# Optimization experiments

Measured on AMD Instinct MI355X. Metric: run time of the kernel, lower is better.

Reference implementation:

```python
import jax, jax.numpy as jnp
import numpy as np

B, N, K = 32, 64, 128          # batch, atoms per cell, channel width (128x0e + 128x1o)
R_MAX = 5.0
NUM_BESSEL = 8
P_CUT = 5                       # num_polynomial_cutoff
AVG_NEIGH = 16.0                # avg_num_neighbors
H_MLP = 512                     # hidden_dimensions_size, n_hidden_dimensions = 2
FEAT = 5 * K                    # ((num_interactions-1)*4 + 1) * 128 = 640


def silu(x):
    return x * jax.nn.sigmoid(x)


def _bessel_cutoff(r, mask):
    # Bessel radial basis * polynomial cutoff (MACE), masked on valid edges.
    n = jnp.arange(1, NUM_BESSEL + 1, dtype=r.dtype)
    rb = jnp.sqrt(2.0 / R_MAX) * jnp.sin(n * (jnp.pi / R_MAX) * r[..., None]) / r[..., None]
    u = r / R_MAX
    p = float(P_CUT)
    fc = 1.0 - 0.5 * (p + 1) * (p + 2) * u**P_CUT + p * (p + 2) * u**(P_CUT + 1) - 0.5 * p * (p + 1) * u**(P_CUT + 2)
    fc = fc * (u < 1.0)
    return rb * (fc * mask)[..., None]


def _sph(uvec):
    # Real spherical harmonics l=0,1,2 (component normalization), uvec: unit edge vectors.
    x, y, z = uvec[..., 0], uvec[..., 1], uvec[..., 2]
    s3, s5, s15 = 3.0**0.5, 5.0**0.5, 15.0**0.5
    Y0 = jnp.ones_like(x)[..., None]
    Y1 = jnp.stack([s3 * x, s3 * y, s3 * z], -1)
    Y2 = jnp.stack([s15 * x * y, s15 * y * z, 0.5 * s5 * (3 * z * z - 1.0),
                    s15 * x * z, 0.5 * s15 * (x * x - y * y)], -1)
    return Y0, Y1, Y2


def _radial_mlp(x, w0, b0, w1, b1, w2, b2, w3, b3):
    h = silu(x @ w0 + b0)
    h = silu(h @ w1 + b1)
    h = silu(h @ w2 + b2)
    return h @ w3 + b3


def setup_inputs() -> dict:
    key = jax.random.key(0)
    ks = jax.random.split(key, 32)
    f32 = jnp.float32

    def lin(k, fan_in, shape):
        return (jax.random.normal(k, shape, dtype=f32) / np.sqrt(fan_in)).astype(f32)

    inp = {
        "noisy_relative_positions": jax.random.uniform(ks[0], (B, N, 3), dtype=f32),
        "time": jax.random.uniform(ks[1], (B, 1), dtype=f32),
        "unit_cell": (11.0 * jnp.eye(3, dtype=f32) + 0.3 * jax.random.uniform(ks[2], (B, 3, 3), dtype=f32)),
        "w_embed": lin(ks[3], 1, (K,)),
        # interaction 1 radial MLP: 8 -> 64 -> 64 -> 64 -> 3*K (weights for l=0,1,2 paths)
        "r1_w0": lin(ks[4], NUM_BESSEL, (NUM_BESSEL, 64)), "r1_b0": jnp.zeros((64,), f32),
        "r1_w1": lin(ks[5], 64, (64, 64)), "r1_b1": jnp.zeros((64,), f32),
        "r1_w2": lin(ks[6], 64, (64, 64)), "r1_b2": jnp.zeros((64,), f32),
        "r1_w3": lin(ks[7], 64, (64, 3 * K)), "r1_b3": jnp.zeros((3 * K,), f32),
        "mix1_l0": lin(ks[8], K, (K, K)),
        "mix1_l1": lin(ks[9], K, (K, K)),
        "mix1_l2": lin(ks[10], K, (K, K)),
        # interaction 2 radial MLP: 8 -> 64 -> 64 -> 64 -> 2*K (paths 0e x 0e -> 0e, 1o x 1o -> 0e)
        "r2_w0": lin(ks[11], NUM_BESSEL, (NUM_BESSEL, 64)), "r2_b0": jnp.zeros((64,), f32),
        "r2_w1": lin(ks[12], 64, (64, 64)), "r2_b1": jnp.zeros((64,), f32),
        "r2_w2": lin(ks[13], 64, (64, 64)), "r2_b2": jnp.zeros((64,), f32),
        "r2_w3": lin(ks[14], 64, (64, 2 * K)), "r2_b3": jnp.zeros((2 * K,), f32),
        "mix2": lin(ks[15], K, (K, K)),
        # readout MLP: 641 -> 512 -> 512 -> 3
        "mlp_w0": lin(ks[16], FEAT + 1, (FEAT + 1, H_MLP)), "mlp_b0": jnp.zeros((H_MLP,), f32),
        "mlp_w1": lin(ks[17], H_MLP, (H_MLP, H_MLP)), "mlp_b1": jnp.zeros((H_MLP,), f32),
        "mlp_w2": lin(ks[18], H_MLP, (H_MLP, 3)), "mlp_b2": jnp.zeros((3,), f32),
    }
    return inp


def reference(noisy_relative_positions, time, unit_cell, w_embed,
              r1_w0, r1_b0, r1_w1, r1_b1, r1_w2, r1_b2, r1_w3, r1_b3,
              mix1_l0, mix1_l1, mix1_l2,
              r2_w0, r2_b0, r2_w1, r2_b1, r2_w2, r2_b2, r2_w3, r2_b3, mix2,
              mlp_w0, mlp_b0, mlp_w1, mlp_b1, mlp_w2, mlp_b2):
    frac = noisy_relative_positions                      # [B,N,3] fractional
    d = frac[:, :, None, :] - frac[:, None, :, :]        # [B,N,N,3]
    d = d - jnp.round(d)                                 # minimum-image PBC
    dc = jnp.einsum('bijc,bcd->bijd', d, unit_cell)      # cartesian displacements
    r = jnp.sqrt(jnp.maximum(jnp.sum(dc * dc, -1), 1e-12))
    mask = (r < R_MAX) & (~jnp.eye(N, dtype=bool))[None]
    r_safe = jnp.where(mask, r, 1.0)
    uvec = dc / r_safe[..., None] * mask[..., None]      # unit edge vectors (0 off-edge)

    rad = _bessel_cutoff(r_safe, mask)                   # [B,N,N,8]
    Y0, Y1, Y2 = _sph(uvec)                              # [B,N,N,1|3|5]

    h0 = jnp.broadcast_to(w_embed, (B, N, K))            # element embedding (single species)

    # ---- interaction 1: radial-weighted tensor product h_j (x) Y_l, scatter over j ----
    we = _radial_mlp(rad, r1_w0, r1_b0, r1_w1, r1_b1, r1_w2, r1_b2, r1_w3, r1_b3)
    we = we.reshape(B, N, N, 3, K) * mask[..., None, None]
    hj = h0[:, None, :, :]                               # sender features [B,1,N,K]
    msg0 = jnp.einsum('bijk,bijm->bimk', we[..., 0, :] * hj, Y0)[:, :, 0] / AVG_NEIGH  # [B,N,K]
    msg1 = jnp.einsum('bijk,bijm->bimk', we[..., 1, :] * hj, Y1) / AVG_NEIGH           # [B,N,3,K]
    msg2 = jnp.einsum('bijk,bijm->bimk', we[..., 2, :] * hj, Y2) / AVG_NEIGH           # [B,N,5,K]

    s1 = msg0 @ mix1_l0 + jnp.sum(msg2 * msg2, axis=2) @ mix1_l2   # scalars [B,N,K]
    v1 = jnp.einsum('bimk,kc->bimc', msg1, mix1_l1)                # vectors [B,N,3,K]
    h1 = silu(s1)

    # ---- interaction 2: scalar output from 0e x 0e and 1o x 1o -> 0e paths ----
    we2 = _radial_mlp(rad, r2_w0, r2_b0, r2_w1, r2_b1, r2_w2, r2_b2, r2_w3, r2_b3)
    we2 = we2.reshape(B, N, N, 2, K) * mask[..., None, None]
    msg_a = jnp.sum(we2[..., 0, :] * h1[:, None, :, :], axis=2)    # [B,N,K]
    inv = jnp.einsum('bijm,bjmk->bijk', Y1, v1)                    # Y1 . v1_j invariant
    msg_b = jnp.sum(we2[..., 1, :] * inv, axis=2)
    s2 = ((msg_a + msg_b) / AVG_NEIGH) @ mix2                      # [B,N,K]

    # node_feats: layer1 full irreps (128x0e + 128x1o -> 512) + layer2 scalars (128) = 640
    node_feats = jnp.concatenate([s1, v1.reshape(B, N, 3 * K), s2], axis=-1)

    t = jnp.broadcast_to(time[:, None, :], (B, N, 1))
    x = jnp.concatenate([node_feats, t], axis=-1)                  # [B,N,641]
    x = jax.nn.relu(x @ mlp_w0 + mlp_b0)
    x = jax.nn.relu(x @ mlp_w1 + mlp_b1)
    return x @ mlp_w2 + mlp_b2                                     # [B,N,3]
```

## Files before the change

### kernel.cpp

```cpp
#include <hip/hip_runtime.h>
#include <math.h>

#define B_ 32
#define N_ 64
#define K_ 128
#define NPAIR (B_*N_*N_)

typedef __attribute__((ext_vector_type(8))) short short8;
typedef __attribute__((ext_vector_type(8))) __bf16 bf16x8;
typedef __attribute__((ext_vector_type(4))) float floatx4;

__device__ __forceinline__ float silu_f(float x) {
    return x / (1.0f + expf(-x));
}
__device__ __forceinline__ float4 ld4(const float* p) { return *(const float4*)p; }

__device__ __forceinline__ short f2bf(float x) {
    union { float f; unsigned u; } v; v.f = x;
    unsigned r = (v.u + 0x7FFFu + ((v.u >> 16) & 1u)) >> 16;
    return (short)r;
}
__device__ __forceinline__ float bf2f(short s) {
    union { unsigned u; float f; } v;
    v.u = ((unsigned)(unsigned short)s) << 16;
    return v.f;
}
__device__ __forceinline__ bf16x8 ld_frag(const short* p) {
    short8 r = *(const short8*)p;
    return __builtin_bit_cast(bf16x8, r);
}

__global__ __launch_bounds__(256) void prep_kernel(
    const float* __restrict__ r1w0, const float* __restrict__ r1w1,
    const float* __restrict__ r1w2, const float* __restrict__ r1w3,
    const float* __restrict__ r2w0, const float* __restrict__ r2w1,
    const float* __restrict__ r2w2, const float* __restrict__ r2w3,
    const float* __restrict__ r2b3,
    const float* __restrict__ mw0, const float* __restrict__ mw1,
    const float* __restrict__ wemb,
    const float* __restrict__ l0, const float* __restrict__ l1,
    const float* __restrict__ l2, const float* __restrict__ mix2,
    short* __restrict__ dst)
{
    int idx = blockIdx.x * 256 + threadIdx.x;
    if (idx >= 757760) return;
    short v;
    if (idx < 4096) {
        int n = idx >> 6, k = idx & 63; v = f2bf(r1w1[k*64 + n]);
    } else if (idx < 8192) {
        int i = idx - 4096; int n = i >> 6, k = i & 63; v = f2bf(r1w2[k*64 + n]);
    } else if (idx < 12288) {
        int i = idx - 8192; int n = i >> 6, k = i & 63; v = f2bf(r2w1[k*64 + n]);
    } else if (idx < 16384) {
        int i = idx - 12288; int n = i >> 6, k = i & 63; v = f2bf(r2w2[k*64 + n]);
    } else if (idx < 40960) {
        int i = idx - 16384; int col = i / 96, k = i - col*96;
        v = (k < 64) ? f2bf(r2w3[k*256 + col])
          : (k == 64) ? f2bf(r2b3[col]) : (short)0;
    } else if (idx < 401408) {
        int i = idx - 40960; int n = i / 704, k = i - n*704;
        v = (k < 641) ? f2bf(mw0[(size_t)k*512 + n]) : (short)0;
    } else if (idx < 663552) {
        int i = idx - 401408; int n = i >> 9, k = i & 511;
        v = f2bf(mw1[(size_t)k*512 + n]);
    } else if (idx < 665600) {
        int i = idx - 663552; int n = i >> 5, k = i & 31;
        v = (k < 8) ? f2bf(r1w0[k*64 + n]) : (short)0;
    } else if (idx < 667648) {
        int i = idx - 665600; int n = i >> 5, k = i & 31;
        v = (k < 8) ? f2bf(r2w0[k*64 + n]) : (short)0;
    } else if (idx < 692224) {
        int i = idx - 667648; int col = i >> 6, h = i & 63;
        v = f2bf(r1w3[h*384 + col] * wemb[col & 127] * 0.0625f);
    } else if (idx < 741376) {
        int i = idx - 692224; int n = i / 384, k = i - n*384;
        float f;
        if (k < 128)       f = l0[k*128 + n];
        else if (k < 256)  f = l2[(k-128)*128 + n];
        else               f = l1[(k-256)*128 + n];
        v = f2bf(f);
    } else {
        int i = idx - 741376; int n = i >> 7, k = i & 127;
        v = f2bf(mix2[k*128 + n] * 0.0625f);
    }
    dst[idx] = v;
}

__global__ __launch_bounds__(256) void geom_kernel(
    const float* __restrict__ pos, const float* __restrict__ cell,
    short* __restrict__ radbf, float* __restrict__ Y1, float* __restrict__ Y2,
    float* __restrict__ maskf)
{
    int p = blockIdx.x * 256 + threadIdx.x;
    if (p >= NPAIR) return;
    int b = p >> 12;
    int ij = p & 4095;
    int i = ij >> 6, j = ij & 63;
    const float* pi = pos + (size_t)(b*N_ + i)*3;
    const float* pj = pos + (size_t)(b*N_ + j)*3;
    float d0 = pi[0]-pj[0], d1 = pi[1]-pj[1], d2 = pi[2]-pj[2];
    d0 -= rintf(d0); d1 -= rintf(d1); d2 -= rintf(d2);
    const float* C = cell + b*9;
    float dc0 = d0*C[0] + d1*C[3] + d2*C[6];
    float dc1 = d0*C[1] + d1*C[4] + d2*C[7];
    float dc2 = d0*C[2] + d1*C[5] + d2*C[8];
    float r2 = fmaxf(dc0*dc0 + dc1*dc1 + dc2*dc2, 1e-12f);
    float r = sqrtf(r2);
    bool m = (r < 5.0f) && (i != j);
    float mf = m ? 1.0f : 0.0f;
    float rs = m ? r : 1.0f;
    float inv_rs = 1.0f / rs;
    float x = dc0*inv_rs*mf, y = dc1*inv_rs*mf, z = dc2*inv_rs*mf;
    float u = r * 0.2f;
    float u2 = u*u, u4 = u2*u2, u5 = u4*u;
    float fc = 1.0f - 21.0f*u5 + 35.0f*u5*u - 15.0f*u5*u2;
    fc = (u < 1.0f) ? fc : 0.0f;
    float pref = 0.6324555320336759f * inv_rs * (fc * mf);
    float w = 0.6283185307179586f * rs;
    float sw = sinf(w), cw = cosf(w);
    float c2 = 2.0f * cw;
    short8 sv;
    float sp = 0.f, s = sw;
    #pragma unroll
    for (int n = 0; n < 8; n++) {
        sv[n] = f2bf(pref * s);
        float ns = c2*s - sp;
        sp = s; s = ns;
    }
    *(short8*)&radbf[(size_t)p*8] = sv;
    const float s3  = 1.7320508075688772f;
    const float s5  = 2.23606797749979f;
    const float s15 = 3.872983346207417f;
    float* y1 = Y1 + (size_t)p*3;
    y1[0] = s3*x; y1[1] = s3*y; y1[2] = s3*z;
    float* y2 = Y2 + (size_t)p*5;
    y2[0] = s15*x*y;
    y2[1] = s15*y*z;
    y2[2] = 0.5f*s5*(3.0f*z*z - 1.0f);
    y2[3] = s15*x*z;
    y2[4] = 0.5f*s15*(x*x - y*y);
    maskf[p] = mf;
}

__global__ __launch_bounds__(256) void bigmlp_kernel(
    const short* __restrict__ radbf,
    const short* __restrict__ w0T1, const float* __restrict__ b01,
    const short* __restrict__ w1T1, const float* __restrict__ b11,
    const short* __restrict__ w2T1, const float* __restrict__ b21,
    short* __restrict__ hc1,
    const short* __restrict__ w0T2, const float* __restrict__ b02,
    const short* __restrict__ w1T2, const float* __restrict__ b12,
    const short* __restrict__ w2T2, const float* __restrict__ b22,
    short* __restrict__ hc2)
{
    __shared__ short radB[128*40];
    __shared__ short actA[128*72];
    __shared__ short actB[128*72];
    int t = threadIdx.x;
    int wv = t >> 6, lane = t & 63, qd = lane >> 4, nn = lane & 15;
    size_t p0 = (size_t)blockIdx.x * 128;

    if (t < 128) {
        uint4 rv = *(const uint4*)&radbf[(p0 + t)*8];
        uint4 z = {0,0,0,0};
        *(uint4*)&radB[t*40]      = rv;
        *(uint4*)&radB[t*40 + 8]  = z;
        *(uint4*)&radB[t*40 + 16] = z;
        *(uint4*)&radB[t*40 + 24] = z;
        *(uint4*)&radB[t*40 + 32] = z;
    }
    __syncthreads();

    const short* w0Ts[2] = {w0T1, w0T2};
    const short* w1Ts[2] = {w1T1, w1T2};
    const short* w2Ts[2] = {w2T1, w2T2};
    const float* b0s[2]  = {b01, b02};
    const float* b1s[2]  = {b11, b12};
    const float* b2s[2]  = {b21, b22};
    short* hcs[2] = {hc1, hc2};

    for (int net = 0; net < 2; net++) {
        const short* w0T = w0Ts[net];
        const short* w1T = w1Ts[net];
        const short* w2T = w2Ts[net];
        const float* b0 = b0s[net];
        const float* b1 = b1s[net];
        const float* b2 = b2s[net];
        short* hc = hcs[net];
        #pragma unroll
        for (int ms = 0; ms < 2; ms++) {
            int r0 = wv*32 + ms*16;
            bf16x8 a = ld_frag(&radB[(r0 + nn)*40 + qd*8]);
            #pragma unroll
            for (int tt = 0; tt < 4; tt++) {
                floatx4 acc = (floatx4){0.f,0.f,0.f,0.f};
                bf16x8 bb = ld_frag(&w0T[(tt*16 + nn)*32 + qd*8]);
                acc = __builtin_amdgcn_mfma_f32_16x16x32_bf16(a, bb, acc, 0, 0, 0);
                int col = tt*16 + nn;
                float bv = b0[col];
                #pragma unroll
                for (int i = 0; i < 4; i++)
                    actA[(r0 + qd*4 + i)*72 + col] = f2bf(silu_f(acc[i] + bv));
            }
        }
        __syncthreads();
        #pragma unroll
        for (int ms = 0; ms < 2; ms++) {
            int r0 = wv*32 + ms*16;
            bf16x8 a0 = ld_frag(&actA[(r0 + nn)*72 + qd*8]);
            bf16x8 a1 = ld_frag(&actA[(r0 + nn)*72 + 32 + qd*8]);
            #pragma unroll
            for (int tt = 0; tt < 4; tt++) {
                floatx4 acc = (floatx4){0.f,0.f,0.f,0.f};
                bf16x8 b0f = ld_frag(&w1T[(tt*16 + nn)*64 + qd*8]);
                bf16x8 b1f = ld_frag(&w1T[(tt*16 + nn)*64 + 32 + qd*8]);
                acc = __builtin_amdgcn_mfma_f32_16x16x32_bf16(a0, b0f, acc, 0, 0, 0);
                acc = __builtin_amdgcn_mfma_f32_16x16x32_bf16(a1, b1f, acc, 0, 0, 0);
                int col = tt*16 + nn;
                float bv = b1[col];
                #pragma unroll
                for (int i = 0; i < 4; i++)
                    actB[(r0 + qd*4 + i)*72 + col] = f2bf(silu_f(acc[i] + bv));
            }
        }
        __syncthreads();
        #pragma unroll
        for (int ms = 0; ms < 2; ms++) {
            int r0 = wv*32 + ms*16;
            bf16x8 a0 = ld_frag(&actB[(r0 + nn)*72 + qd*8]);
            bf16x8 a1 = ld_frag(&actB[(r0 + nn)*72 + 32 + qd*8]);
            #pragma unroll
            for (int tt = 0; tt < 4; tt++) {
                floatx4 acc = (floatx4){0.f,0.f,0.f,0.f};
                bf16x8 b0f = ld_frag(&w2T[(tt*16 + nn)*64 + qd*8]);
                bf16x8 b1f = ld_frag(&w2T[(tt*16 + nn)*64 + 32 + qd*8]);
                acc = __builtin_amdgcn_mfma_f32_16x16x32_bf16(a0, b0f, acc, 0, 0, 0);
                acc = __builtin_amdgcn_mfma_f32_16x16x32_bf16(a1, b1f, acc, 0, 0, 0);
                int col = tt*16 + nn;
                float bv = b2[col];
                #pragma unroll
                for (int i = 0; i < 4; i++)
                    hc[(p0 + r0 + qd*4 + i)*64 + col] = f2bf(silu_f(acc[i] + bv));
            }
        }
    }
}

__global__ __launch_bounds__(256) void msg1_kernel(
    const short* __restrict__ hc1, const float* __restrict__ Y1g,
    const float* __restrict__ Y2g, const float* __restrict__ maskg,
    const float* __restrict__ wemb, const float* __restrict__ b3,
    const short* __restrict__ w3T, const short* __restrict__ lT,
    const float* __restrict__ timeg,
    short* __restrict__ h1bf, float* __restrict__ v1g, short* __restrict__ featsb)
{
    __shared__ __align__(16) char pool[19008];
    short* hcT  = (short*)pool;
    short* A2   = (short*)pool;
    short* YmB  = (short*)(pool + 9216);
    short* GB   = (short*)(pool + 11520);
    float* msgF = (float*)(pool + 13824);
    float* qF   = (float*)(pool + 18432);
    float* SY   = (float*)(pool + 18944);

    int t = threadIdx.x;
    int wv = t >> 6, lane = t & 63, qd = lane >> 4, nn = lane & 15;
    int node = blockIdx.x;
    int b = node >> 6;
    size_t pbase = (size_t)node * 64;

    for (int idx = t; idx < 512; idx += 256) {
        int j = idx >> 3, h0 = (idx & 7)*8;
        short8 v = *(const short8*)&hc1[((size_t)node*64 + j)*64 + h0];
        #pragma unroll
        for (int q = 0; q < 8; q++) hcT[(h0 + q)*72 + j] = v[q];
    }
    for (int idx = t; idx < 1152; idx += 256) YmB[idx] = 0;
    __syncthreads();
    if (t < 64) {
        int j = t;
        float mf = maskg[pbase + j];
        YmB[j] = f2bf(mf);
        #pragma unroll
        for (int m = 0; m < 3; m++) YmB[(1+m)*72 + j] = f2bf(Y1g[(pbase+j)*3 + m] * mf);
        #pragma unroll
        for (int m = 0; m < 5; m++) YmB[(4+m)*72 + j] = f2bf(Y2g[(pbase+j)*5 + m] * mf);
    }
    __syncthreads();
    if (t < 16) {
        float acc = 0.f;
        if (t < 9) for (int j = 0; j < 64; j++) acc += bf2f(YmB[t*72 + j]);
        SY[t] = acc;
    }
    {
        floatx4 accG = (floatx4){0.f,0.f,0.f,0.f};
        #pragma unroll
        for (int ks = 0; ks < 64; ks += 32) {
            bf16x8 a = ld_frag(&YmB[nn*72 + ks + qd*8]);
            bf16x8 bfr = ld_frag(&hcT[(wv*16 + nn)*72 + ks + qd*8]);
            accG = __builtin_amdgcn_mfma_f32_16x16x32_bf16(a, bfr, accG, 0, 0, 0);
        }
        #pragma unroll
        for (int i = 0; i < 4; i++)
            GB[(qd*4 + i)*72 + wv*16 + nn] = f2bf(accG[i]);
    }
    __syncthreads();
    {
        bf16x8 a0f = ld_frag(&GB[nn*72 + 0  + qd*8]);
        bf16x8 a1f = ld_frag(&GB[nn*72 + 32 + qd*8]);
        #pragma unroll
        for (int tl = 0; tl < 6; tl++) {
            int col0 = (wv*6 + tl)*16;
            floatx4 acc = (floatx4){0.f,0.f,0.f,0.f};
            bf16x8 b0f = ld_frag(&w3T[(col0 + nn)*64 + 0  + qd*8]);
            bf16x8 b1f = ld_frag(&w3T[(col0 + nn)*64 + 32 + qd*8]);
            acc = __builtin_amdgcn_mfma_f32_16x16x32_bf16(a0f, b0f, acc, 0, 0, 0);
            acc = __builtin_amdgcn_mfma_f32_16x16x32_bf16(a1f, b1f, acc, 0, 0, 0);
            int col = col0 + nn;
            int csec = col >> 7, k = col & 127;
            #pragma unroll
            for (int i = 0; i < 4; i++) {
                int m = qd*4 + i;
                bool valid = (csec == 0) ? (m == 0)
                           : (csec == 1) ? (m >= 1 && m <= 3)
                                         : (m >= 4 && m <= 8);
                if (valid)
                    msgF[m*128 + k] = acc[i] + SY[m]*b3[col]*wemb[k]*0.0625f;
            }
        }
    }
    __syncthreads();
    if (t < 128) {
        float acc = 0.f;
        #pragma unroll
        for (int m = 4; m < 9; m++) { float v = msgF[m*128 + t]; acc += v*v; }
        qF[t] = acc;
    }
    __syncthreads();
    for (int idx = t; idx < 6272; idx += 256) A2[idx] = 0;
    __syncthreads();
    A2[t] = (t < 128) ? f2bf(msgF[t]) : f2bf(qF[t - 128]);
    if (t < 128) {
        #pragma unroll
        for (int m = 1; m <= 3; m++)
            A2[m*392 + 256 + t] = f2bf(msgF[m*128 + t]);
    }
    __syncthreads();
    #pragma unroll
    for (int tt = 0; tt < 2; tt++) {
        int col = (wv*2 + tt)*16 + nn;
        floatx4 acc = (floatx4){0.f,0.f,0.f,0.f};
        #pragma unroll
        for (int ks = 0; ks < 384; ks += 32) {
            bf16x8 a = ld_frag(&A2[nn*392 + ks + qd*8]);
            bf16x8 bfr = ld_frag(&lT[(size_t)col*384 + ks + qd*8]);
            acc = __builtin_amdgcn_mfma_f32_16x16x32_bf16(a, bfr, acc, 0, 0, 0);
        }
        if (qd == 0) {
            float s1 = acc[0];
            featsb[(size_t)node*704 + col] = f2bf(s1);
            h1bf[(size_t)node*128 + col] = f2bf(silu_f(s1));
            #pragma unroll
            for (int i = 1; i < 4; i++) {
                float v = acc[i];
                v1g[(size_t)node*384 + (i-1)*128 + col] = v;
                featsb[(size_t)node*704 + 128 + (i-1)*128 + col] = f2bf(v);
            }
        }
    }
    if (t == 0) featsb[(size_t)node*704 + 640] = f2bf(timeg[b]);
    if (t < 63) featsb[(size_t)node*704 + 641 + t] = 0;
}

__global__ __launch_bounds__(256) void msg2_kernel(
    const short* __restrict__ hc2, const float* __restrict__ Y1g,
    const float* __restrict__ maskg, const short* __restrict__ w3extT,
    const short* __restrict__ h1bf, const float* __restrict__ v1g,
    short* __restrict__ msgabf)
{
    __shared__ __align__(16) char pool[50688];
    short* hc2e  = (short*)pool;
    short* h1B   = (short*)(pool + 14336);
    short* invB  = (short*)(pool + 31744);
    float* Y1s   = (float*)(pool + 49152);
    float* msgab = (float*)(pool + 50176);

    int t = threadIdx.x;
    int wv = t >> 6, lane = t & 63, qd = lane >> 4, nn = lane & 15;
    int node = blockIdx.x;
    int b = node >> 6;
    size_t pbase = (size_t)node * 64;

    if (t < 64) {
        int j = t;
        #pragma unroll
        for (int m = 0; m < 3; m++) Y1s[j*4 + m] = Y1g[(pbase+j)*3 + m];
        float mf = maskg[pbase + j];
        short8 z8 = {0,0,0,0,0,0,0,0};
        *(short8*)&hc2e[j*112 + 64] = z8;
        *(short8*)&hc2e[j*112 + 72] = z8;
        *(short8*)&hc2e[j*112 + 80] = z8;
        *(short8*)&hc2e[j*112 + 88] = z8;
        *(short8*)&hc2e[j*112 + 96] = z8;
        *(short8*)&hc2e[j*112 + 104] = z8;
        hc2e[j*112 + 64] = f2bf(mf);
    }
    for (int idx = t; idx < 512; idx += 256) {
        int j = idx >> 3, h0 = (idx & 7)*8;
        short8 v = *(const short8*)&hc2[((size_t)node*64 + j)*64 + h0];
        float mf = maskg[pbase + j];
        if (mf == 0.f) { short8 z8 = {0,0,0,0,0,0,0,0}; v = z8; }
        *(short8*)&hc2e[j*112 + h0] = v;
    }
    for (int idx = t; idx < 1024; idx += 256) {
        int j = idx >> 4, k0 = (idx & 15)*8;
        *(uint4*)&h1B[j*136 + k0] = *(const uint4*)&h1bf[((size_t)b*64 + j)*128 + k0];
    }
    if (t < 128) msgab[t] = 0.f;
    __syncthreads();
    for (int idx = t; idx < 2048; idx += 256) {
        int j = idx >> 5, kq = (idx & 31)*4;
        const float* vb = &v1g[((size_t)b*64 + j)*384 + kq];
        float4 vx = ld4(vb), vy = ld4(vb + 128), vz = ld4(vb + 256);
        float yx = Y1s[j*4+0], yy = Y1s[j*4+1], yz = Y1s[j*4+2];
        invB[j*136 + kq + 0] = f2bf(yx*vx.x + yy*vy.x + yz*vz.x);
        invB[j*136 + kq + 1] = f2bf(yx*vx.y + yy*vy.y + yz*vz.y);
        invB[j*136 + kq + 2] = f2bf(yx*vx.z + yy*vy.z + yz*vz.z);
        invB[j*136 + kq + 3] = f2bf(yx*vx.w + yy*vy.w + yz*vz.w);
    }
    __syncthreads();
    {
        bf16x8 a0 = ld_frag(&hc2e[(wv*16 + nn)*112 + 0  + qd*8]);
        bf16x8 a1 = ld_frag(&hc2e[(wv*16 + nn)*112 + 32 + qd*8]);
        bf16x8 a2 = ld_frag(&hc2e[(wv*16 + nn)*112 + 64 + qd*8]);
        for (int g = 0; g < 4; g++) {
            #pragma unroll
            for (int tt = 0; tt < 4; tt++) {
                int col0 = g*64 + tt*16;
                floatx4 acc = (floatx4){0.f,0.f,0.f,0.f};
                bf16x8 b0f = ld_frag(&w3extT[(col0 + nn)*96 + 0  + qd*8]);
                bf16x8 b1f = ld_frag(&w3extT[(col0 + nn)*96 + 32 + qd*8]);
                bf16x8 b2f = ld_frag(&w3extT[(col0 + nn)*96 + 64 + qd*8]);
                acc = __builtin_amdgcn_mfma_f32_16x16x32_bf16(a0, b0f, acc, 0, 0, 0);
                acc = __builtin_amdgcn_mfma_f32_16x16x32_bf16(a1, b1f, acc, 0, 0, 0);
                acc = __builtin_amdgcn_mfma_f32_16x16x32_bf16(a2, b2f, acc, 0, 0, 0);
                int col = col0 + nn;
                int k = col & 127;
                const short* src = (col < 128) ? h1B : invB;
                float p = 0.f;
                #pragma unroll
                for (int i = 0; i < 4; i++) {
                    int j = wv*16 + qd*4 + i;
                    p += acc[i] * bf2f(src[j*136 + k]);
                }
                p += __shfl_xor(p, 16);
                p += __shfl_xor(p, 32);
                if (qd == 0) atomicAdd(&msgab[k], p);
            }
        }
    }
    __syncthreads();
    if (t < 128) msgabf[(size_t)node*128 + t] = f2bf(msgab[t]);
}

__global__ __launch_bounds__(64) void s2_kernel(
    const short* __restrict__ msgabf, const short* __restrict__ mix2T,
    short* __restrict__ featsb)
{
    int lane = threadIdx.x, qd = lane >> 4, nn = lane & 15;
    int m0 = blockIdx.x * 16, n0 = blockIdx.y * 64;
    floatx4 acc[4];
    #pragma unroll
    for (int tt = 0; tt < 4; tt++) acc[tt] = (floatx4){0.f,0.f,0.f,0.f};
    #pragma unroll
    for (int ks = 0; ks < 128; ks += 32) {
        bf16x8 a = ld_frag(&msgabf[(size_t)(m0 + nn)*128 + ks + qd*8]);
        #pragma unroll
        for (int tt = 0; tt < 4; tt++) {
            bf16x8 bb = ld_frag(&mix2T[(size_t)(n0 + tt*16 + nn)*128 + ks + qd*8]);
            acc[tt] = __builtin_amdgcn_mfma_f32_16x16x32_bf16(a, bb, acc[tt], 0, 0, 0);
        }
    }
    #pragma unroll
    for (int tt = 0; tt < 4; tt++) {
        int n = n0 + tt*16 + nn;
        #pragma unroll
        for (int i = 0; i < 4; i++) {
            int m = m0 + qd*4 + i;
            featsb[(size_t)m*704 + 512 + n] = f2bf(acc[tt][i]);
        }
    }
}

__global__ __launch_bounds__(256) void gemm_part_kernel(
    const short* __restrict__ A, int lda,
    const short* __restrict__ BT, int ldb,
    int ngran, int nsplit, float* __restrict__ Cp)
{
    int t = threadIdx.x;
    int wv = t >> 6, lane = t & 63, qd = lane >> 4, nn = lane & 15;
    int m0 = blockIdx.x * 64, n0 = blockIdx.y * 64, z = blockIdx.z;
    int g0 = (z*ngran)/nsplit, g1 = ((z+1)*ngran)/nsplit;
    floatx4 acc[4];
    #pragma unroll
    for (int tt = 0; tt < 4; tt++) acc[tt] = (floatx4){0.f,0.f,0.f,0.f};
    int row = wv*16 + nn;
    for (int g = g0; g < g1; g++) {
        int k = g*32;
        bf16x8 a = ld_frag(&A[(size_t)(m0 + row)*lda + k + qd*8]);
        #pragma unroll
        for (int tt = 0; tt < 4; tt++) {
            bf16x8 bb = ld_frag(&BT[(size_t)(n0 + tt*16 + nn)*ldb + k + qd*8]);
            acc[tt] = __builtin_amdgcn_mfma_f32_16x16x32_bf16(a, bb, acc[tt], 0, 0, 0);
        }
    }
    float* out = Cp + (size_t)z*2048*512;
    #pragma unroll
    for (int tt = 0; tt < 4; tt++) {
        int n = n0 + tt*16 + nn;
        #pragma unroll
        for (int i = 0; i < 4; i++)
            out[(size_t)(m0 + wv*16 + qd*4 + i)*512 + n] = acc[tt][i];
    }
}

__global__ __launch_bounds__(256) void combine_kernel(
    const float* __restrict__ Cp, const float* __restrict__ bias,
    short* __restrict__ out)
{
    int idx = (blockIdx.x * 256 + threadIdx.x) * 4;
    int n = idx & 511;
    float4 s = ld4(&Cp[idx]);
    #pragma unroll
    for (int z = 1; z < 4; z++) {
        float4 p = ld4(&Cp[(size_t)z*1048576 + idx]);
        s.x += p.x; s.y += p.y; s.z += p.z; s.w += p.w;
    }
    float4 bv = ld4(&bias[n]);
    short4 o;
    o.x = f2bf(fmaxf(s.x + bv.x, 0.f));
    o.y = f2bf(fmaxf(s.y + bv.y, 0.f));
    o.z = f2bf(fmaxf(s.z + bv.z, 0.f));
    o.w = f2bf(fmaxf(s.w + bv.w, 0.f));
    *(short4*)&out[idx] = o;
}

__global__ __launch_bounds__(64) void final3_kernel(
    const short* __restrict__ H, const float* __restrict__ w2,
    const float* __restrict__ b2, float* __restrict__ out)
{
    int node = blockIdx.x, lane = threadIdx.x;
    float a0 = 0.f, a1 = 0.f, a2 = 0.f;
    #pragma unroll
    for (int r = 0; r < 8; r++) {
        int k = r*64 + lane;
        float h = bf2f(H[(size_t)node*512 + k]);
        a0 += h * w2[k*3 + 0];
        a1 += h * w2[k*3 + 1];
        a2 += h * w2[k*3 + 2];
    }
    #pragma unroll
    for (int off = 32; off > 0; off >>= 1) {
        a0 += __shfl_down(a0, off);
        a1 += __shfl_down(a1, off);
        a2 += __shfl_down(a2, off);
    }
    if (lane == 0) {
        out[(size_t)node*3 + 0] = a0 + b2[0];
        out[(size_t)node*3 + 1] = a1 + b2[1];
        out[(size_t)node*3 + 2] = a2 + b2[2];
    }
}

extern "C" void kernel_launch(void* const* d_in, const int* in_sizes, int n_in,
                              void* d_out, int out_size, void* d_ws, size_t ws_size,
                              hipStream_t stream) {
    const float* pos   = (const float*)d_in[0];
    const float* timeg = (const float*)d_in[1];
    const float* cell  = (const float*)d_in[2];
    const float* wemb  = (const float*)d_in[3];
    const float* r1w0  = (const float*)d_in[4];
    const float* r1b0  = (const float*)d_in[5];
    const float* r1w1  = (const float*)d_in[6];
    const float* r1b1  = (const float*)d_in[7];
    const float* r1w2  = (const float*)d_in[8];
    const float* r1b2  = (const float*)d_in[9];
    const float* r1w3  = (const float*)d_in[10];
    const float* r1b3  = (const float*)d_in[11];
    const float* l0    = (const float*)d_in[12];
    const float* l1    = (const float*)d_in[13];
    const float* l2    = (const float*)d_in[14];
    const float* r2w0  = (const float*)d_in[15];
    const float* r2b0  = (const float*)d_in[16];
    const float* r2w1  = (const float*)d_in[17];
    const float* r2b1  = (const float*)d_in[18];
    const float* r2w2  = (const float*)d_in[19];
    const float* r2b2  = (const float*)d_in[20];
    const float* r2w3  = (const float*)d_in[21];
    const float* r2b3  = (const float*)d_in[22];
    const float* mix2  = (const float*)d_in[23];
    const float* mw0   = (const float*)d_in[24];
    const float* mb0   = (const float*)d_in[25];
    const float* mw1   = (const float*)d_in[26];
    const float* mb1   = (const float*)d_in[27];
    const float* mw2   = (const float*)d_in[28];
    const float* mb2   = (const float*)d_in[29];

    float* ws = (float*)d_ws;
    short* radbf  = (short*)ws;
    float* Y1     = ws + 524288;
    float* Y2     = ws + 917504;
    float* maskf  = ws + 1572864;
    float* v1     = ws + 1703936;
    short* featsb = (short*)(ws + 2490368);
    short* prep   = (short*)(ws + 3211264);
    short* hc1    = (short*)(ws + 3590144);
    short* hc2    = (short*)(ws + 7784448);
    short* h1bf   = (short*)(ws + 11978752);
    short* msgabf = (short*)(ws + 12109824);

    short* w1T_1  = prep;
    short* w2T_1  = prep + 4096;
    short* w1T_2  = prep + 8192;
    short* w2T_2  = prep + 12288;
    short* w3extT = prep + 16384;
    short* wT0    = prep + 40960;
    short* wT1    = prep + 401408;
    short* w0T_1  = prep + 663552;
    short* w0T_2  = prep + 665600;
    short* w3T_1  = prep + 667648;
    short* lT     = prep + 692224;
    short* mix2T  = prep + 741376;

    float* Cp   = (float*)hc1;
    short* h0bb = radbf;
    short* h1bb = (short*)Y2;

    prep_kernel<<<(757760 + 255)/256, 256, 0, stream>>>(
        r1w0, r1w1, r1w2, r1w3, r2w0, r2w1, r2w2, r2w3, r2b3,
        mw0, mw1, wemb, l0, l1, l2, mix2, prep);
    geom_kernel<<<NPAIR/256, 256, 0, stream>>>(pos, cell, radbf, Y1, Y2, maskf);
    bigmlp_kernel<<<NPAIR/128, 256, 0, stream>>>(radbf,
        w0T_1, r1b0, w1T_1, r1b1, w2T_1, r1b2, hc1,
        w0T_2, r2b0, w1T_2, r2b1, w2T_2, r2b2, hc2);
    msg1_kernel<<<B_*N_, 256, 0, stream>>>(hc1, Y1, Y2, maskf, wemb, r1b3,
        w3T_1, lT, timeg, h1bf, v1, featsb);
    msg2_kernel<<<B_*N_, 256, 0, stream>>>(hc2, Y1, maskf, w3extT, h1bf, v1,
        msgabf);
    {
        dim3 g(128, 2);
        s2_kernel<<<g, 64, 0, stream>>>(msgabf, mix2T, featsb);
    }
    {
        dim3 g(32, 8, 4);
        gemm_part_kernel<<<g, 256, 0, stream>>>(featsb, 704, wT0, 704, 22, 4, Cp);
        combine_kernel<<<1024, 256, 0, stream>>>(Cp, mb0, h0bb);
        gemm_part_kernel<<<g, 256, 0, stream>>>(h0bb, 512, wT1, 512, 16, 4, Cp);
        combine_kernel<<<1024, 256, 0, stream>>>(Cp, mb1, h1bb);
    }
    final3_kernel<<<B_*N_, 64, 0, stream>>>(h1bb, mw2, mb2, (float*)d_out);
}
```

Before: 322.0 us.

## Exploit pair symmetry, merge geom into prep, fold s2 into msg2

Geometry is computed only for the upper triangle of atom pairs (i<=j), and the mirrored entries are written with Y1 negated and Y2, mask and radial features reused. The radial-MLP kernel now processes only the 2080 triangular pairs per cell and scatters each hidden row to both (i,j) and (j,i). The geometry and weight-prep kernels are merged into one launch. The s2 GEMM kernel is removed in favour of a scalar dot-product loop at the end of msg2, and silu/sin/cos/rcp switch to fast AMD intrinsics. This roughly halves the radial-MLP work and drops two launches, at the cost of scattered writes and a serial 128-step loop per thread in msg2.

```diff
diff --git a/kernel.cpp b/kernel.cpp
--- a/kernel.cpp
+++ b/kernel.cpp
@@ -5,13 +5,18 @@
 #define N_ 64
 #define K_ 128
 #define NPAIR (B_*N_*N_)
+#define NTRI 2080
+#define GEOM_BLOCKS 260
+#define PREP_COUNT 741376
+#define PREP_BLOCKS 2896
 
 typedef __attribute__((ext_vector_type(8))) short short8;
 typedef __attribute__((ext_vector_type(8))) __bf16 bf16x8;
 typedef __attribute__((ext_vector_type(4))) float floatx4;
 
 __device__ __forceinline__ float silu_f(float x) {
-    return x / (1.0f + expf(-x));
+    float e = __builtin_amdgcn_exp2f(-1.442695040888963f * x);
+    return x * __builtin_amdgcn_rcpf(1.0f + e);
 }
 __device__ __forceinline__ float4 ld4(const float* p) { return *(const float4*)p; }
 
@@ -30,7 +35,22 @@
     return __builtin_bit_cast(bf16x8, r);
 }
 
-__global__ __launch_bounds__(256) void prep_kernel(
+__device__ __forceinline__ int2 tri_decode(int t) {
+    float f = (129.0f - sqrtf((float)(16641 - 8*t))) * 0.5f;
+    int i = (int)f;
+    int off = 64*i - (i*(i-1))/2;
+    if (off > t) { i--; off = 64*i - (i*(i-1))/2; }
+    else {
+        int offn = 64*(i+1) - ((i+1)*i)/2;
+        if (offn <= t) { i = i+1; off = offn; }
+    }
+    return make_int2(i, i + (t - off));
+}
+
+__global__ __launch_bounds__(256) void pre_kernel(
+    const float* __restrict__ pos, const float* __restrict__ cell,
+    short* __restrict__ radbf, float* __restrict__ Y1, float* __restrict__ Y2,
+    float* __restrict__ maskf,
     const float* __restrict__ r1w0, const float* __restrict__ r1w1,
     const float* __restrict__ r1w2, const float* __restrict__ r1w3,
     const float* __restrict__ r2w0, const float* __restrict__ r2w1,
@@ -39,11 +59,66 @@
     const float* __restrict__ mw0, const float* __restrict__ mw1,
     const float* __restrict__ wemb,
     const float* __restrict__ l0, const float* __restrict__ l1,
-    const float* __restrict__ l2, const float* __restrict__ mix2,
-    short* __restrict__ dst)
+    const float* __restrict__ l2, short* __restrict__ dst)
 {
-    int idx = blockIdx.x * 256 + threadIdx.x;
-    if (idx >= 757760) return;
+    int t = threadIdx.x;
+    if (blockIdx.x < GEOM_BLOCKS) {
+        int gt = blockIdx.x * 256 + t;
+        int b = gt / NTRI;
+        int tt = gt - b*NTRI;
+        int2 ij = tri_decode(tt);
+        int i = ij.x, j = ij.y;
+        const float* pi = pos + (size_t)(b*N_ + i)*3;
+        const float* pj = pos + (size_t)(b*N_ + j)*3;
+        float d0 = pi[0]-pj[0], d1 = pi[1]-pj[1], d2 = pi[2]-pj[2];
+        d0 -= rintf(d0); d1 -= rintf(d1); d2 -= rintf(d2);
+        const float* C = cell + b*9;
+        float dc0 = d0*C[0] + d1*C[3] + d2*C[6];
+        float dc1 = d0*C[1] + d1*C[4] + d2*C[7];
+        float dc2 = d0*C[2] + d1*C[5] + d2*C[8];
+        float r2 = fmaxf(dc0*dc0 + dc1*dc1 + dc2*dc2, 1e-12f);
+        float r = sqrtf(r2);
+        bool m = (r < 5.0f) && (i != j);
+        float mf = m ? 1.0f : 0.0f;
+        float rs = m ? r : 1.0f;
+        float inv_rs = __builtin_amdgcn_rcpf(rs);
+        inv_rs = inv_rs * (2.0f - rs*inv_rs);
+        float x = dc0*inv_rs*mf, y = dc1*inv_rs*mf, z = dc2*inv_rs*mf;
+        float u = r * 0.2f;
+        float u2 = u*u, u4 = u2*u2, u5 = u4*u;
+        float fc = 1.0f - 21.0f*u5 + 35.0f*u5*u - 15.0f*u5*u2;
+        fc = (u < 1.0f) ? fc : 0.0f;
+        float pref = 0.6324555320336759f * inv_rs * (fc * mf);
+        float rev = 0.1f * rs;
+        float sw = __builtin_amdgcn_sinf(rev);
+        float cw = __builtin_amdgcn_cosf(rev);
+        float c2 = 2.0f * cw;
+        short8 sv;
+        float sp = 0.f, s = sw;
+        #pragma unroll
+        for (int n = 0; n < 8; n++) {
+            sv[n] = f2bf(pref * s);
+            float ns = c2*s - sp;
+            sp = s; s = ns;
+        }
+        size_t pu = ((size_t)b*64 + i)*64 + j;
+        size_t pl = ((size_t)b*64 + j)*64 + i;
+        *(short8*)&radbf[pu*8] = sv;
+        const float s3  = 1.7320508075688772f;
+        const float s5  = 2.23606797749979f;
+        const float s15 = 3.872983346207417f;
+        float y1x = s3*x, y1y = s3*y, y1z = s3*z;
+        Y1[pu*3+0] = y1x; Y1[pu*3+1] = y1y; Y1[pu*3+2] = y1z;
+        Y1[pl*3+0] = -y1x; Y1[pl*3+1] = -y1y; Y1[pl*3+2] = -y1z;
+        float q0 = s15*x*y, q1 = s15*y*z, q2 = 0.5f*s5*(3.0f*z*z - 1.0f);
+        float q3 = s15*x*z, q4 = 0.5f*s15*(x*x - y*y);
+        Y2[pu*5+0]=q0; Y2[pu*5+1]=q1; Y2[pu*5+2]=q2; Y2[pu*5+3]=q3; Y2[pu*5+4]=q4;
+        Y2[pl*5+0]=q0; Y2[pl*5+1]=q1; Y2[pl*5+2]=q2; Y2[pl*5+3]=q3; Y2[pl*5+4]=q4;
+        maskf[pu] = mf; maskf[pl] = mf;
+        return;
+    }
+    int idx = (blockIdx.x - GEOM_BLOCKS) * 256 + t;
+    if (idx >= PREP_COUNT) return;
     short v;
     if (idx < 4096) {
         int n = idx >> 6, k = idx & 63; v = f2bf(r1w1[k*64 + n]);
@@ -72,74 +147,15 @@
     } else if (idx < 692224) {
         int i = idx - 667648; int col = i >> 6, h = i & 63;
         v = f2bf(r1w3[h*384 + col] * wemb[col & 127] * 0.0625f);
-    } else if (idx < 741376) {
+    } else {
         int i = idx - 692224; int n = i / 384, k = i - n*384;
         float f;
         if (k < 128)       f = l0[k*128 + n];
         else if (k < 256)  f = l2[(k-128)*128 + n];
         else               f = l1[(k-256)*128 + n];
         v = f2bf(f);
-    } else {
-        int i = idx - 741376; int n = i >> 7, k = i & 127;
-        v = f2bf(mix2[k*128 + n] * 0.0625f);
     }
     dst[idx] = v;
-}
-
-__global__ __launch_bounds__(256) void geom_kernel(
-    const float* __restrict__ pos, const float* __restrict__ cell,
-    short* __restrict__ radbf, float* __restrict__ Y1, float* __restrict__ Y2,
-    float* __restrict__ maskf)
-{
-    int p = blockIdx.x * 256 + threadIdx.x;
-    if (p >= NPAIR) return;
-    int b = p >> 12;
-    int ij = p & 4095;
-    int i = ij >> 6, j = ij & 63;
-    const float* pi = pos + (size_t)(b*N_ + i)*3;
-    const float* pj = pos + (size_t)(b*N_ + j)*3;
-    float d0 = pi[0]-pj[0], d1 = pi[1]-pj[1], d2 = pi[2]-pj[2];
-    d0 -= rintf(d0); d1 -= rintf(d1); d2 -= rintf(d2);
-    const float* C = cell + b*9;
-    float dc0 = d0*C[0] + d1*C[3] + d2*C[6];
-    float dc1 = d0*C[1] + d1*C[4] + d2*C[7];
-    float dc2 = d0*C[2] + d1*C[5] + d2*C[8];
-    float r2 = fmaxf(dc0*dc0 + dc1*dc1 + dc2*dc2, 1e-12f);
-    float r = sqrtf(r2);
-    bool m = (r < 5.0f) && (i != j);
-    float mf = m ? 1.0f : 0.0f;
-    float rs = m ? r : 1.0f;
-    float inv_rs = 1.0f / rs;
-    float x = dc0*inv_rs*mf, y = dc1*inv_rs*mf, z = dc2*inv_rs*mf;
-    float u = r * 0.2f;
-    float u2 = u*u, u4 = u2*u2, u5 = u4*u;
-    float fc = 1.0f - 21.0f*u5 + 35.0f*u5*u - 15.0f*u5*u2;
-    fc = (u < 1.0f) ? fc : 0.0f;
-    float pref = 0.6324555320336759f * inv_rs * (fc * mf);
-    float w = 0.6283185307179586f * rs;
-    float sw = sinf(w), cw = cosf(w);
-    float c2 = 2.0f * cw;
-    short8 sv;
-    float sp = 0.f, s = sw;
-    #pragma unroll
-    for (int n = 0; n < 8; n++) {
-        sv[n] = f2bf(pref * s);
-        float ns = c2*s - sp;
-        sp = s; s = ns;
-    }
-    *(short8*)&radbf[(size_t)p*8] = sv;
-    const float s3  = 1.7320508075688772f;
-    const float s5  = 2.23606797749979f;
-    const float s15 = 3.872983346207417f;
-    float* y1 = Y1 + (size_t)p*3;
-    y1[0] = s3*x; y1[1] = s3*y; y1[2] = s3*z;
-    float* y2 = Y2 + (size_t)p*5;
-    y2[0] = s15*x*y;
-    y2[1] = s15*y*z;
-    y2[2] = 0.5f*s5*(3.0f*z*z - 1.0f);
-    y2[3] = s15*x*z;
-    y2[4] = 0.5f*s15*(x*x - y*y);
-    maskf[p] = mf;
 }
 
 __global__ __launch_bounds__(256) void bigmlp_kernel(
@@ -156,13 +172,24 @@
     __shared__ short radB[128*40];
     __shared__ short actA[128*72];
     __shared__ short actB[128*72];
+    __shared__ int prs[128];
     int t = threadIdx.x;
     int wv = t >> 6, lane = t & 63, qd = lane >> 4, nn = lane & 15;
-    size_t p0 = (size_t)blockIdx.x * 128;
+    int bb = blockIdx.x / 17;
+    int chunk = blockIdx.x - bb*17;
 
     if (t < 128) {
-        uint4 rv = *(const uint4*)&radbf[(p0 + t)*8];
+        int tt0 = chunk*128 + t;
         uint4 z = {0,0,0,0};
+        uint4 rv = z;
+        int pr = -1;
+        if (tt0 < NTRI) {
+            int2 ij = tri_decode(tt0);
+            pr = (ij.x << 8) | ij.y;
+            size_t pu = ((size_t)bb*64 + ij.x)*64 + ij.y;
+            rv = *(const uint4*)&radbf[pu*8];
+        }
+        prs[t] = pr;
         *(uint4*)&radB[t*40]      = rv;
         *(uint4*)&radB[t*40 + 8]  = z;
         *(uint4*)&radB[t*40 + 16] = z;
@@ -194,8 +221,8 @@
             #pragma unroll
             for (int tt = 0; tt < 4; tt++) {
                 floatx4 acc = (floatx4){0.f,0.f,0.f,0.f};
-                bf16x8 bb = ld_frag(&w0T[(tt*16 + nn)*32 + qd*8]);
-                acc = __builtin_amdgcn_mfma_f32_16x16x32_bf16(a, bb, acc, 0, 0, 0);
+                bf16x8 bb_ = ld_frag(&w0T[(tt*16 + nn)*32 + qd*8]);
+                acc = __builtin_amdgcn_mfma_f32_16x16x32_bf16(a, bb_, acc, 0, 0, 0);
                 int col = tt*16 + nn;
                 float bv = b0[col];
                 #pragma unroll
@@ -239,10 +266,20 @@
                 int col = tt*16 + nn;
                 float bv = b2[col];
                 #pragma unroll
-                for (int i = 0; i < 4; i++)
-                    hc[(p0 + r0 + qd*4 + i)*64 + col] = f2bf(silu_f(acc[i] + bv));
+                for (int i = 0; i < 4; i++) {
+                    int pr = prs[r0 + qd*4 + i];
+                    if (pr >= 0) {
+                        short val = f2bf(silu_f(acc[i] + bv));
+                        int pi = pr >> 8, pj = pr & 255;
+                        size_t base = (size_t)bb*4096;
+                        hc[(base + pi*64 + pj)*64 + col] = val;
+                        if (pi != pj)
+                            hc[(base + pj*64 + pi)*64 + col] = val;
+                    }
+                }
             }
         }
+        __syncthreads();
     }
 }
 
@@ -376,7 +413,7 @@
     const short* __restrict__ hc2, const float* __restrict__ Y1g,
     const float* __restrict__ maskg, const short* __restrict__ w3extT,
     const short* __restrict__ h1bf, const float* __restrict__ v1g,
-    short* __restrict__ msgabf)
+    const float* __restrict__ mix2, short* __restrict__ featsb)
 {
     __shared__ __align__(16) char pool[50688];
     short* hc2e  = (short*)pool;
@@ -460,35 +497,10 @@
         }
     }
     __syncthreads();
-    if (t < 128) msgabf[(size_t)node*128 + t] = f2bf(msgab[t]);
-}
-
-__global__ __launch_bounds__(64) void s2_kernel(
-    const short* __restrict__ msgabf, const short* __restrict__ mix2T,
-    short* __restrict__ featsb)
-{
-    int lane = threadIdx.x, qd = lane >> 4, nn = lane & 15;
-    int m0 = blockIdx.x * 16, n0 = blockIdx.y * 64;
-    floatx4 acc[4];
-    #pragma unroll
-    for (int tt = 0; tt < 4; tt++) acc[tt] = (floatx4){0.f,0.f,0.f,0.f};
-    #pragma unroll
-    for (int ks = 0; ks < 128; ks += 32) {
-        bf16x8 a = ld_frag(&msgabf[(size_t)(m0 + nn)*128 + ks + qd*8]);
-        #pragma unroll
-        for (int tt = 0; tt < 4; tt++) {
-            bf16x8 bb = ld_frag(&mix2T[(size_t)(n0 + tt*16 + nn)*128 + ks + qd*8]);
-            acc[tt] = __builtin_amdgcn_mfma_f32_16x16x32_bf16(a, bb, acc[tt], 0, 0, 0);
-        }
-    }
-    #pragma unroll
-    for (int tt = 0; tt < 4; tt++) {
-        int n = n0 + tt*16 + nn;
-        #pragma unroll
-        for (int i = 0; i < 4; i++) {
-            int m = m0 + qd*4 + i;
-            featsb[(size_t)m*704 + 512 + n] = f2bf(acc[tt][i]);
-        }
+    if (t < 128) {
+        float acc = 0.f;
+        for (int k = 0; k < 128; k++) acc += msgab[k] * mix2[k*128 + t];
+        featsb[(size_t)node*704 + 512 + t] = f2bf(acc * 0.0625f);
     }
 }
 
@@ -617,7 +629,6 @@
     short* hc1    = (short*)(ws + 3590144);
     short* hc2    = (short*)(ws + 7784448);
     short* h1bf   = (short*)(ws + 11978752);
-    short* msgabf = (short*)(ws + 12109824);
 
     short* w1T_1  = prep;
     short* w2T_1  = prep + 4096;
@@ -630,27 +641,22 @@
     short* w0T_2  = prep + 665600;
     short* w3T_1  = prep + 667648;
     short* lT     = prep + 692224;
-    short* mix2T  = prep + 741376;
 
     float* Cp   = (float*)hc1;
     short* h0bb = radbf;
     short* h1bb = (short*)Y2;
 
-    prep_kernel<<<(757760 + 255)/256, 256, 0, stream>>>(
+    pre_kernel<<<GEOM_BLOCKS + PREP_BLOCKS, 256, 0, stream>>>(
+        pos, cell, radbf, Y1, Y2, maskf,
         r1w0, r1w1, r1w2, r1w3, r2w0, r2w1, r2w2, r2w3, r2b3,
-        mw0, mw1, wemb, l0, l1, l2, mix2, prep);
-    geom_kernel<<<NPAIR/256, 256, 0, stream>>>(pos, cell, radbf, Y1, Y2, maskf);
-    bigmlp_kernel<<<NPAIR/128, 256, 0, stream>>>(radbf,
+        mw0, mw1, wemb, l0, l1, l2, prep);
+    bigmlp_kernel<<<32*17, 256, 0, stream>>>(radbf,
         w0T_1, r1b0, w1T_1, r1b1, w2T_1, r1b2, hc1,
         w0T_2, r2b0, w1T_2, r2b1, w2T_2, r2b2, hc2);
     msg1_kernel<<<B_*N_, 256, 0, stream>>>(hc1, Y1, Y2, maskf, wemb, r1b3,
         w3T_1, lT, timeg, h1bf, v1, featsb);
     msg2_kernel<<<B_*N_, 256, 0, stream>>>(hc2, Y1, maskf, w3extT, h1bf, v1,
-        msgabf);
-    {
-        dim3 g(128, 2);
-        s2_kernel<<<g, 64, 0, stream>>>(msgabf, mix2T, featsb);
-    }
+        mix2, featsb);
     {
         dim3 g(32, 8, 4);
         gemm_part_kernel<<<g, 256, 0, stream>>>(featsb, 704, wT0, 704, 22, 4, Cp);
```

After: 301.2 us. 1.07x faster.
